# Performance work log

Hardware: AMD Instinct MI355X
Metric: run time of the kernel (lower is better)

Reference implementation:

```python
import jax, jax.numpy as jnp
import numpy as np

TOKENS, INPUT_DIM, NUM_EXPERTS, TOP_K = 16384, 2048, 64, 2


def setup_inputs() -> dict:
    key = jax.random.key(0)
    k1, k2 = jax.random.split(key)
    x = jax.random.normal(k1, (TOKENS, INPUT_DIM), dtype=jnp.float32)
    # nn.Linear weight is [out, in]; scale like torch default init
    W = jax.random.normal(k2, (NUM_EXPERTS, INPUT_DIM), dtype=jnp.float32) * (1.0 / np.sqrt(INPUT_DIM))
    b = jnp.zeros((NUM_EXPERTS,), dtype=jnp.float32)
    return {"x": x, "W": W, "b": b}


def reference(x, W, b):
    # logits = x @ W.T + b  -> [tokens, num_experts]
    logits = jnp.einsum("td,ed->te", x, W) + b
    top_k_vals, top_k_indices = jax.lax.top_k(logits, TOP_K)
    router_probs = jax.nn.softmax(top_k_vals, axis=1)
    return router_probs, top_k_indices, logits
```

## Files before the change

kernel.cpp:

```cpp
#include <hip/hip_runtime.h>
#include <math.h>

#define TOKENS 16384
#define DIM    2048
#define NE     64
#define TB     32
#define KG     8
#define KW     (DIM / KG)
#define NCH    (KW / 16)

typedef _Float16 f16x8 __attribute__((ext_vector_type(8)));
typedef float    f32x16 __attribute__((ext_vector_type(16)));

__global__ __launch_bounds__(256) void wpack_kernel(const float* __restrict__ W,
                                                    _Float16* __restrict__ wp) {
    const int g  = blockIdx.x * 256 + threadIdx.x;
    const int c  = g >> 7;
    const int eg = (g >> 6) & 1;
    const int l  = g & 63;
    const int e  = eg * 32 + (l & 31);
    const int k0 = c * 16 + (l >> 5) * 8;
    const float* src = W + (size_t)e * DIM + k0;
    float4 a = *(const float4*)src;
    float4 bq = *(const float4*)(src + 4);
    const float* pa = (const float*)&a;
    const float* pb = (const float*)&bq;
    f16x8 h, lo;
    #pragma unroll
    for (int j = 0; j < 4; ++j) {
        _Float16 h1 = (_Float16)pa[j];
        h[j] = h1; lo[j] = (_Float16)(pa[j] - (float)h1);
        _Float16 h2 = (_Float16)pb[j];
        h[4 + j] = h2; lo[4 + j] = (_Float16)(pb[j] - (float)h2);
    }
    _Float16* dst = wp + ((size_t)(c * 2 + eg) * 2) * 512 + l * 8;
    *(f16x8*)dst = h;
    *(f16x8*)(dst + 512) = lo;
}

__global__ __launch_bounds__(512, 4) void router_kernel(const float* __restrict__ x,
                                                        const _Float16* __restrict__ wp,
                                                        const float* __restrict__ b,
                                                        float* __restrict__ out) {
    __shared__ __align__(16) float lds[KG * TB * NE];

    const int tid  = threadIdx.x;
    const int kg   = tid >> 6;
    const int lane = tid & 63;
    const int t0   = blockIdx.x * TB;
    const int m    = lane & 31;
    const int ko   = lane >> 5;

    const float* xp = x + (size_t)(t0 + m) * DIM + kg * KW + ko * 8;
    const _Float16* wpb = wp + (size_t)kg * NCH * 2048;

    f32x16 acc0, acc1;
    #pragma unroll
    for (int i = 0; i < 16; ++i) { acc0[i] = 0.0f; acc1[i] = 0.0f; }

    float4 xs0[2], xs1[2];
    f16x8  bs[2][4];

    auto ld = [&](int c, int sl) {
        const float* s = xp + c * 16;
        xs0[sl] = *(const float4*)s;
        xs1[sl] = *(const float4*)(s + 4);
        const _Float16* wb = wpb + (size_t)c * 2048 + lane * 8;
        bs[sl][0] = *(const f16x8*)(wb);
        bs[sl][1] = *(const f16x8*)(wb + 512);
        bs[sl][2] = *(const f16x8*)(wb + 1024);
        bs[sl][3] = *(const f16x8*)(wb + 1536);
    };

    ld(0, 0);
    ld(1, 1);

    #pragma unroll 2
    for (int c = 0; c < NCH; ++c) {
        const int sl = c & 1;
        f16x8 ah, al;
        {
            const float* p0 = (const float*)&xs0[sl];
            const float* p1 = (const float*)&xs1[sl];
            #pragma unroll
            for (int j = 0; j < 4; ++j) {
                _Float16 h1 = (_Float16)p0[j];
                ah[j] = h1; al[j] = (_Float16)(p0[j] - (float)h1);
                _Float16 h2 = (_Float16)p1[j];
                ah[4 + j] = h2; al[4 + j] = (_Float16)(p1[j] - (float)h2);
            }
        }
        const f16x8 b0h = bs[sl][0], b0l = bs[sl][1];
        const f16x8 b1h = bs[sl][2], b1l = bs[sl][3];

        acc0 = __builtin_amdgcn_mfma_f32_32x32x16_f16(ah, b0h, acc0, 0, 0, 0);
        acc1 = __builtin_amdgcn_mfma_f32_32x32x16_f16(ah, b1h, acc1, 0, 0, 0);
        acc0 = __builtin_amdgcn_mfma_f32_32x32x16_f16(ah, b0l, acc0, 0, 0, 0);
        acc1 = __builtin_amdgcn_mfma_f32_32x32x16_f16(ah, b1l, acc1, 0, 0, 0);
        acc0 = __builtin_amdgcn_mfma_f32_32x32x16_f16(al, b0h, acc0, 0, 0, 0);
        acc1 = __builtin_amdgcn_mfma_f32_32x32x16_f16(al, b1h, acc1, 0, 0, 0);

        if (c + 2 < NCH) ld(c + 2, sl);
    }

    float* zone = lds + kg * (TB * NE);
    #pragma unroll
    for (int r = 0; r < 16; ++r) {
        const int row = (r & 3) + 8 * (r >> 2) + 4 * ko;
        zone[row * 64 + m]      = acc0[r];
        zone[row * 64 + 32 + m] = acc1[r];
    }
    __syncthreads();

    float* logits_out = out + (size_t)TOKENS * 4;
    {
        const int row = tid >> 4;
        const int c4  = (tid & 15) * 4;
        const int base = row * 64 + c4;
        float4 s0 = *(float4*)&lds[base];
        #pragma unroll
        for (int z = 1; z < KG; ++z) {
            float4 a0 = *(float4*)&lds[z * 2048 + base];
            s0.x += a0.x; s0.y += a0.y; s0.z += a0.z; s0.w += a0.w;
        }
        float4 bv0 = *(const float4*)&b[c4];
        s0.x += bv0.x; s0.y += bv0.y; s0.z += bv0.z; s0.w += bv0.w;
        *(float4*)&lds[base] = s0;
        *(float4*)&logits_out[(size_t)(t0 + row) * 64 + c4] = s0;
    }
    __syncthreads();

    float* idxf = out + (size_t)TOKENS * 2;
    for (int i = 0; i < 4; ++i) {
        const int t = kg * 4 + i;
        const float v = lds[t * 64 + lane];

        float v1 = v; int i1 = lane;
        #pragma unroll
        for (int off = 32; off >= 1; off >>= 1) {
            float ov = __shfl_xor(v1, off, 64);
            int   oi = __shfl_xor(i1, off, 64);
            if (ov > v1 || (ov == v1 && oi < i1)) { v1 = ov; i1 = oi; }
        }
        float vm = (lane == i1) ? -INFINITY : v;
        float v2 = vm; int i2 = lane;
        #pragma unroll
        for (int off = 32; off >= 1; off >>= 1) {
            float ov = __shfl_xor(v2, off, 64);
            int   oi = __shfl_xor(i2, off, 64);
            if (ov > v2 || (ov == v2 && oi < i2)) { v2 = ov; i2 = oi; }
        }

        if (lane == 0) {
            const int tok = t0 + t;
            float e1 = expf(v2 - v1);
            float sden = 1.0f + e1;
            *(float2*)&out[(size_t)tok * 2]  = make_float2(1.0f / sden, e1 / sden);
            *(float2*)&idxf[(size_t)tok * 2] = make_float2((float)i1, (float)i2);
        }
    }
}

extern "C" void kernel_launch(void* const* d_in, const int* in_sizes, int n_in,
                              void* d_out, int out_size, void* d_ws, size_t ws_size,
                              hipStream_t stream) {
    const float* x = (const float*)d_in[0];
    const float* W = (const float*)d_in[1];
    const float* b = (const float*)d_in[2];
    float* out = (float*)d_out;
    _Float16* wp = (_Float16*)d_ws;

    wpack_kernel<<<64, 256, 0, stream>>>(W, wp);
    router_kernel<<<TOKENS / TB, 512, 0, stream>>>(x, wp, b, out);
}
```

Measured before the change: 207.2 us.

## Stage x tiles through double-buffered LDS with async global_load_lds and swizzle

```diff
diff --git a/kernel.cpp b/kernel.cpp
--- a/kernel.cpp
+++ b/kernel.cpp
@@ -6,8 +6,8 @@
 #define NE     64
 #define TB     32
 #define KG     8
-#define KW     (DIM / KG)
-#define NCH    (KW / 16)
+#define BK     256
+#define NSTEP  (DIM / BK)
 
 typedef _Float16 f16x8 __attribute__((ext_vector_type(8)));
 typedef float    f32x16 __attribute__((ext_vector_type(16)));
@@ -42,7 +42,7 @@
                                                         const _Float16* __restrict__ wp,
                                                         const float* __restrict__ b,
                                                         float* __restrict__ out) {
-    __shared__ __align__(16) float lds[KG * TB * NE];
+    __shared__ __align__(16) float lds[16384];
 
     const int tid  = threadIdx.x;
     const int kg   = tid >> 6;
@@ -51,37 +51,66 @@
     const int m    = lane & 31;
     const int ko   = lane >> 5;
 
-    const float* xp = x + (size_t)(t0 + m) * DIM + kg * KW + ko * 8;
-    const _Float16* wpb = wp + (size_t)kg * NCH * 2048;
-
-    f32x16 acc0, acc1;
-    #pragma unroll
-    for (int i = 0; i < 16; ++i) { acc0[i] = 0.0f; acc1[i] = 0.0f; }
-
-    float4 xs0[2], xs1[2];
-    f16x8  bs[2][4];
-
-    auto ld = [&](int c, int sl) {
-        const float* s = xp + c * 16;
-        xs0[sl] = *(const float4*)s;
-        xs1[sl] = *(const float4*)(s + 4);
-        const _Float16* wb = wpb + (size_t)c * 2048 + lane * 8;
+    const float* xbase = x + (size_t)t0 * DIM;
+    auto stage = [&](int s, int bsel) {
+        #pragma unroll
+        for (int i = 0; i < 4; ++i) {
+            const int r = kg * 4 + i;
+            const float* src = xbase + (size_t)r * DIM + s * BK + ((lane ^ r) << 2);
+            float* dst = lds + bsel * 8192 + r * 256;
+            __builtin_amdgcn_global_load_lds(
+                (const __attribute__((address_space(1))) void*)src,
+                (__attribute__((address_space(3))) void*)dst,
+                16, 0, 0);
+        }
+    };
+
+    int roff[2][2];
+    #pragma unroll
+    for (int cc = 0; cc < 2; ++cc)
+        #pragma unroll
+        for (int q = 0; q < 2; ++q) {
+            const int g = kg * 8 + cc * 4 + ko * 2 + q;
+            roff[cc][q] = m * 1024 + ((g ^ m) << 4);
+        }
+
+    const _Float16* wpl = wp + lane * 8;
+    f16x8 bs[2][4];
+    auto wld = [&](int n, int sl) {
+        const int C = ((n >> 1) << 4) + (kg << 1) + (n & 1);
+        const _Float16* wb = wpl + (size_t)C * 2048;
         bs[sl][0] = *(const f16x8*)(wb);
         bs[sl][1] = *(const f16x8*)(wb + 512);
         bs[sl][2] = *(const f16x8*)(wb + 1024);
         bs[sl][3] = *(const f16x8*)(wb + 1536);
     };
 
-    ld(0, 0);
-    ld(1, 1);
+    f32x16 acc0, acc1;
+    #pragma unroll
+    for (int i = 0; i < 16; ++i) { acc0[i] = 0.0f; acc1[i] = 0.0f; }
+
+    stage(0, 0);
+    wld(0, 0); wld(1, 1);
+    __syncthreads();
 
     #pragma unroll 2
-    for (int c = 0; c < NCH; ++c) {
-        const int sl = c & 1;
-        f16x8 ah, al;
-        {
-            const float* p0 = (const float*)&xs0[sl];
-            const float* p1 = (const float*)&xs1[sl];
+    for (int s = 0; s < NSTEP; ++s) {
+        const int bsel = s & 1;
+        if (s + 1 < NSTEP) stage(s + 1, bsel ^ 1);
+
+        const char* lb = (const char*)lds + bsel * 32768;
+        float4 xv[2][2];
+        #pragma unroll
+        for (int cc = 0; cc < 2; ++cc) {
+            xv[cc][0] = *(const float4*)(lb + roff[cc][0]);
+            xv[cc][1] = *(const float4*)(lb + roff[cc][1]);
+        }
+
+        #pragma unroll
+        for (int cc = 0; cc < 2; ++cc) {
+            f16x8 ah, al;
+            const float* p0 = (const float*)&xv[cc][0];
+            const float* p1 = (const float*)&xv[cc][1];
             #pragma unroll
             for (int j = 0; j < 4; ++j) {
                 _Float16 h1 = (_Float16)p0[j];
@@ -89,18 +118,20 @@
                 _Float16 h2 = (_Float16)p1[j];
                 ah[4 + j] = h2; al[4 + j] = (_Float16)(p1[j] - (float)h2);
             }
-        }
-        const f16x8 b0h = bs[sl][0], b0l = bs[sl][1];
-        const f16x8 b1h = bs[sl][2], b1l = bs[sl][3];
-
-        acc0 = __builtin_amdgcn_mfma_f32_32x32x16_f16(ah, b0h, acc0, 0, 0, 0);
-        acc1 = __builtin_amdgcn_mfma_f32_32x32x16_f16(ah, b1h, acc1, 0, 0, 0);
-        acc0 = __builtin_amdgcn_mfma_f32_32x32x16_f16(ah, b0l, acc0, 0, 0, 0);
-        acc1 = __builtin_amdgcn_mfma_f32_32x32x16_f16(ah, b1l, acc1, 0, 0, 0);
-        acc0 = __builtin_amdgcn_mfma_f32_32x32x16_f16(al, b0h, acc0, 0, 0, 0);
-        acc1 = __builtin_amdgcn_mfma_f32_32x32x16_f16(al, b1h, acc1, 0, 0, 0);
-
-        if (c + 2 < NCH) ld(c + 2, sl);
+            const f16x8 b0h = bs[cc][0], b0l = bs[cc][1];
+            const f16x8 b1h = bs[cc][2], b1l = bs[cc][3];
+
+            acc0 = __builtin_amdgcn_mfma_f32_32x32x16_f16(ah, b0h, acc0, 0, 0, 0);
+            acc1 = __builtin_amdgcn_mfma_f32_32x32x16_f16(ah, b1h, acc1, 0, 0, 0);
+            acc0 = __builtin_amdgcn_mfma_f32_32x32x16_f16(ah, b0l, acc0, 0, 0, 0);
+            acc1 = __builtin_amdgcn_mfma_f32_32x32x16_f16(ah, b1l, acc1, 0, 0, 0);
+            acc0 = __builtin_amdgcn_mfma_f32_32x32x16_f16(al, b0h, acc0, 0, 0, 0);
+            acc1 = __builtin_amdgcn_mfma_f32_32x32x16_f16(al, b1h, acc1, 0, 0, 0);
+
+            const int n = s * 2 + cc;
+            if (n + 2 < 16) wld(n + 2, cc);
+        }
+        __syncthreads();
     }
 
     float* zone = lds + kg * (TB * NE);
```

After: 200.0 us. 3.5% less time.

## Stage x tiles into LDS via async global_load_lds with 4-deep swizzled pipeline

Applied to the files above, without the earlier changes.

```diff
diff --git a/kernel.cpp b/kernel.cpp
--- a/kernel.cpp
+++ b/kernel.cpp
@@ -6,8 +6,8 @@
 #define NE     64
 #define TB     32
 #define KG     8
-#define KW     (DIM / KG)
-#define NCH    (KW / 16)
+#define BK     128
+#define NSTEP  (DIM / BK)
 
 typedef _Float16 f16x8 __attribute__((ext_vector_type(8)));
 typedef float    f32x16 __attribute__((ext_vector_type(16)));
@@ -42,7 +42,7 @@
                                                         const _Float16* __restrict__ wp,
                                                         const float* __restrict__ b,
                                                         float* __restrict__ out) {
-    __shared__ __align__(16) float lds[KG * TB * NE];
+    __shared__ __align__(16) float lds[16384];
 
     const int tid  = threadIdx.x;
     const int kg   = tid >> 6;
@@ -51,57 +51,92 @@
     const int m    = lane & 31;
     const int ko   = lane >> 5;
 
-    const float* xp = x + (size_t)(t0 + m) * DIM + kg * KW + ko * 8;
-    const _Float16* wpb = wp + (size_t)kg * NCH * 2048;
+    const float* xbase = x + (size_t)t0 * DIM;
+    const _Float16* wpl = wp + lane * 8;
 
     f32x16 acc0, acc1;
     #pragma unroll
     for (int i = 0; i < 16; ++i) { acc0[i] = 0.0f; acc1[i] = 0.0f; }
 
-    float4 xs0[2], xs1[2];
-    f16x8  bs[2][4];
-
-    auto ld = [&](int c, int sl) {
-        const float* s = xp + c * 16;
-        xs0[sl] = *(const float4*)s;
-        xs1[sl] = *(const float4*)(s + 4);
-        const _Float16* wb = wpb + (size_t)c * 2048 + lane * 8;
-        bs[sl][0] = *(const f16x8*)(wb);
-        bs[sl][1] = *(const f16x8*)(wb + 512);
-        bs[sl][2] = *(const f16x8*)(wb + 1024);
-        bs[sl][3] = *(const f16x8*)(wb + 1536);
-    };
-
-    ld(0, 0);
-    ld(1, 1);
-
-    #pragma unroll 2
-    for (int c = 0; c < NCH; ++c) {
-        const int sl = c & 1;
-        f16x8 ah, al;
-        {
-            const float* p0 = (const float*)&xs0[sl];
-            const float* p1 = (const float*)&xs1[sl];
-            #pragma unroll
-            for (int j = 0; j < 4; ++j) {
-                _Float16 h1 = (_Float16)p0[j];
-                ah[j] = h1; al[j] = (_Float16)(p0[j] - (float)h1);
-                _Float16 h2 = (_Float16)p1[j];
-                ah[4 + j] = h2; al[4 + j] = (_Float16)(p1[j] - (float)h2);
-            }
-        }
-        const f16x8 b0h = bs[sl][0], b0l = bs[sl][1];
-        const f16x8 b1h = bs[sl][2], b1l = bs[sl][3];
-
-        acc0 = __builtin_amdgcn_mfma_f32_32x32x16_f16(ah, b0h, acc0, 0, 0, 0);
-        acc1 = __builtin_amdgcn_mfma_f32_32x32x16_f16(ah, b1h, acc1, 0, 0, 0);
-        acc0 = __builtin_amdgcn_mfma_f32_32x32x16_f16(ah, b0l, acc0, 0, 0, 0);
-        acc1 = __builtin_amdgcn_mfma_f32_32x32x16_f16(ah, b1l, acc1, 0, 0, 0);
-        acc0 = __builtin_amdgcn_mfma_f32_32x32x16_f16(al, b0h, acc0, 0, 0, 0);
-        acc1 = __builtin_amdgcn_mfma_f32_32x32x16_f16(al, b1h, acc1, 0, 0, 0);
-
-        if (c + 2 < NCH) ld(c + 2, sl);
-    }
+    f16x8 bs[2][4];
+
+    const int gq  = kg * 4 + ko * 2;
+    const int ro0 = m * 512 + (((gq + 0) ^ (m & 7)) << 4);
+    const int ro1 = m * 512 + (((gq + 1) ^ (m & 7)) << 4);
+
+#define STAGE(S) do {                                                            \
+        _Pragma("unroll")                                                        \
+        for (int i_ = 0; i_ < 2; ++i_) {                                         \
+            const int rp_ = 4 * kg + 2 * i_;                                     \
+            const int r_  = rp_ + (lane >> 5);                                   \
+            const int sg_ = (lane & 31) ^ (r_ & 7);                              \
+            const float* src_ = xbase + (size_t)r_ * DIM + (S) * BK + (sg_ << 2);\
+            float* dst_ = lds + ((S) & 3) * 4096 + rp_ * 128;                    \
+            __builtin_amdgcn_global_load_lds(                                    \
+                (const __attribute__((address_space(1))) void*)src_,             \
+                (__attribute__((address_space(3))) void*)dst_, 16, 0, 0);        \
+        } } while (0)
+
+#define WLD(S) do {                                                              \
+        const _Float16* wb_ = wpl + (size_t)((S) * 8 + kg) * 2048;               \
+        bs[(S) & 1][0] = *(const f16x8*)(wb_);                                   \
+        bs[(S) & 1][1] = *(const f16x8*)(wb_ + 512);                             \
+        bs[(S) & 1][2] = *(const f16x8*)(wb_ + 1024);                            \
+        bs[(S) & 1][3] = *(const f16x8*)(wb_ + 1536);                            \
+    } while (0)
+
+#define COMP(S) do {                                                             \
+        const char* lb_ = (const char*)lds + ((S) & 3) * 16384;                  \
+        float4 xv0_ = *(const float4*)(lb_ + ro0);                               \
+        float4 xv1_ = *(const float4*)(lb_ + ro1);                               \
+        f16x8 ah_, al_;                                                          \
+        const float* p0_ = (const float*)&xv0_;                                  \
+        const float* p1_ = (const float*)&xv1_;                                  \
+        _Pragma("unroll")                                                        \
+        for (int j_ = 0; j_ < 4; ++j_) {                                         \
+            _Float16 h1_ = (_Float16)p0_[j_];                                    \
+            ah_[j_] = h1_; al_[j_] = (_Float16)(p0_[j_] - (float)h1_);           \
+            _Float16 h2_ = (_Float16)p1_[j_];                                    \
+            ah_[4 + j_] = h2_; al_[4 + j_] = (_Float16)(p1_[j_] - (float)h2_);   \
+        }                                                                        \
+        acc0 = __builtin_amdgcn_mfma_f32_32x32x16_f16(ah_, bs[(S)&1][0], acc0, 0, 0, 0); \
+        acc1 = __builtin_amdgcn_mfma_f32_32x32x16_f16(ah_, bs[(S)&1][2], acc1, 0, 0, 0); \
+        acc0 = __builtin_amdgcn_mfma_f32_32x32x16_f16(ah_, bs[(S)&1][1], acc0, 0, 0, 0); \
+        acc1 = __builtin_amdgcn_mfma_f32_32x32x16_f16(ah_, bs[(S)&1][3], acc1, 0, 0, 0); \
+        acc0 = __builtin_amdgcn_mfma_f32_32x32x16_f16(al_, bs[(S)&1][0], acc0, 0, 0, 0); \
+        acc1 = __builtin_amdgcn_mfma_f32_32x32x16_f16(al_, bs[(S)&1][2], acc1, 0, 0, 0); \
+    } while (0)
+
+#define STEP(S, VMC) do {                                                        \
+        WLD((S) + 1);                                                            \
+        if ((S) + 3 < NSTEP) STAGE((S) + 3);                                     \
+        COMP(S);                                                                 \
+        asm volatile("s_waitcnt vmcnt(" VMC ")" ::: "memory");                   \
+        __builtin_amdgcn_s_barrier();                                            \
+    } while (0)
+
+    STAGE(0);
+    asm volatile("" ::: "memory");
+    WLD(0);
+    asm volatile("" ::: "memory");
+    STAGE(1);
+    STAGE(2);
+    asm volatile("s_waitcnt vmcnt(8)" ::: "memory");
+    __builtin_amdgcn_s_barrier();
+
+    STEP(0, "8");  STEP(1, "8");  STEP(2, "8");  STEP(3, "8");
+    STEP(4, "8");  STEP(5, "8");  STEP(6, "8");  STEP(7, "8");
+    STEP(8, "8");  STEP(9, "8");  STEP(10, "8"); STEP(11, "8");
+    STEP(12, "8");
+    STEP(13, "6");
+    STEP(14, "4");
+    COMP(15);
+    __syncthreads();
+
+#undef STEP
+#undef COMP
+#undef WLD
+#undef STAGE
 
     float* zone = lds + kg * (TB * NE);
     #pragma unroll
```

Result: faster. 199.1 us (-3.9%).
